# Optimization experiments

Measured on AMD Instinct MI355X. Metric: run time of the kernel, lower is better.

The kernel has to match this reference:

```python
import jax, jax.numpy as jnp
import numpy as np


def setup_inputs() -> dict:
    key = jax.random.key(0)
    B, C, A, P, N = 4, 1, 180, 384, 256
    sinogram = jax.random.normal(key, (B, C, A, P), dtype=jnp.float32)
    # projection angles uniformly covering [0, pi)
    thetas = jnp.linspace(0.0, np.pi, A, endpoint=False).astype(jnp.float32)
    # uniformly spaced detector positions centered at 0, unit spacing
    positions = jnp.arange(P, dtype=jnp.float32) - (P - 1) / 2.0
    return {"sinogram": sinogram, "thetas": thetas, "positions": positions, "image_size": N}


def reference(sinogram, thetas, positions, image_size):
    """Radon backprojection: image[y,x] = sum_a interp(sinogram[a], x*cos+y*sin)."""
    B, C, A, P = sinogram.shape
    N = image_size
    # pixel-center coordinates, image centered at origin (y axis pointing up)
    c = jnp.arange(N, dtype=sinogram.dtype) - (N - 1) / 2.0
    xs = c[None, :]          # [1, N]
    ys = -c[:, None]         # [N, 1]
    cos = jnp.cos(thetas)[:, None, None]  # [A, 1, 1]
    sin = jnp.sin(thetas)[:, None, None]
    t = xs[None] * cos + ys[None] * sin   # [A, N, N] detector coordinate per (angle, pixel)
    # fractional index into the (uniform) detector position grid
    dp = positions[1] - positions[0]
    f = (t - positions[0]) / dp           # [A, N, N]
    i0 = jnp.floor(f)
    w = f - i0                            # linear interpolation weight
    valid = (i0 >= 0) & (i0 <= P - 2)     # rays falling inside the detector
    i0c = jnp.clip(i0, 0, P - 2).astype(jnp.int32)
    idx = i0c.reshape(A, N * N)[None, None]          # [1, 1, A, N*N]
    v0 = jnp.take_along_axis(sinogram, idx, axis=3)  # [B, C, A, N*N]
    v1 = jnp.take_along_axis(sinogram, idx + 1, axis=3)
    wf = w.reshape(A, N * N)[None, None]
    vm = valid.reshape(A, N * N)[None, None]
    val = jnp.where(vm, v0 * (1.0 - wf) + v1 * wf, 0.0)
    return val.sum(axis=2).reshape(B, C, N, N)
```

## Files before the change

### kernel.cpp

```cpp
#include <hip/hip_runtime.h>
#include <hip/hip_fp16.h>
#include <cmath>


#define ACHUNKS 8
#define MAXPE   512

__global__ __launch_bounds__(256) void radon_pack(
    const float* __restrict__ sino,
    const float* __restrict__ thetas,
    const float* __restrict__ positions,
    uint4* __restrict__ packed,
    float2* __restrict__ trig,
    int A, int P, int PE, int bstride)
{
    const int idx = blockIdx.x * 256 + threadIdx.x;
    const int a = idx / PE;
    const int i = idx - a * PE;
    if (a >= A) return;

    const float p0     = positions[0];
    const float inv_dp = 1.0f / (positions[1] - p0);
    if (i == 0) {
        float th = thetas[a];
        trig[a] = make_float2(cosf(th) * inv_dp, sinf(th) * inv_dp);
        if (a == 0) trig[A] = make_float2(-p0 * inv_dp, 0.0f);
    }

    const int i0 = min(i, P - 1);
    const int i1 = min(i + 1, P - 1);
    const float* s = sino + (size_t)a * P;

    uint4 e;
    unsigned* ep = (unsigned*)&e;
#pragma unroll
    for (int b = 0; b < 4; ++b) {
        const float* sb = s + (size_t)b * bstride;
        __half2 h = __floats2half2_rn(sb[i0], sb[i1]);
        ep[b] = *(const unsigned*)&h;
    }
    packed[(size_t)a * PE + i] = e;
}

__global__ __launch_bounds__(256) void radon_partial_gg(
    const uint4* __restrict__ packed,
    const float2* __restrict__ trig,
    float* __restrict__ part,
    int A, int P, int PE, int N, int chunk)
{
    const int tid = threadIdx.x;
    const int nn  = N * N;
    const int pix = blockIdx.x * 256 + tid;
    const int a0  = blockIdx.y * chunk;
    const int cnt = min(A, a0 + chunk) - a0;

    const int x = pix % N;
    const int y = pix / N;
    const float half = (float)(N - 1) * 0.5f;
    const float cx = (float)x - half;
    const float cy = half - (float)y;
    const float q0 = trig[A].x;

    float acc0 = 0.f, acc1 = 0.f, acc2 = 0.f, acc3 = 0.f;

#pragma unroll 4
    for (int i = 0; i < cnt; ++i) {
        const int a = a0 + i;
        float2 t  = trig[a];
        float f   = fmaf(cx, t.x, fmaf(cy, t.y, q0));
        float i0f = floorf(f);
        int   i0  = (int)i0f;
        float w   = f - i0f;
        float m   = (i0 >= 0 && i0 <= P - 2) ? 1.0f : 0.0f;
        int   ic  = min(max(i0, 0), P - 2);
        float wm  = w * m;
        float om  = m - wm;

        uint4 e = packed[(size_t)a * PE + ic];
        const __half2* hp = (const __half2*)&e;
        float2 g0 = __half22float2(hp[0]);
        float2 g1 = __half22float2(hp[1]);
        float2 g2 = __half22float2(hp[2]);
        float2 g3 = __half22float2(hp[3]);
        acc0 = fmaf(om, g0.x, fmaf(wm, g0.y, acc0));
        acc1 = fmaf(om, g1.x, fmaf(wm, g1.y, acc1));
        acc2 = fmaf(om, g2.x, fmaf(wm, g2.y, acc2));
        acc3 = fmaf(om, g3.x, fmaf(wm, g3.y, acc3));
    }

    if (pix < nn) {
        float* pp = part + (size_t)blockIdx.y * 4 * nn + pix;
        pp[0]              = acc0;
        pp[(size_t)nn]     = acc1;
        pp[(size_t)2 * nn] = acc2;
        pp[(size_t)3 * nn] = acc3;
    }
}

__global__ __launch_bounds__(256) void radon_reduce_kernel(
    const float4* __restrict__ part,
    float4* __restrict__ out,
    int BN4, int nchunks)
{
    int i = blockIdx.x * blockDim.x + threadIdx.x;
    if (i >= BN4) return;
    float4 s = make_float4(0.f, 0.f, 0.f, 0.f);
    for (int c = 0; c < nchunks; ++c) {
        float4 v = part[(size_t)c * BN4 + i];
        s.x += v.x; s.y += v.y; s.z += v.z; s.w += v.w;
    }
    out[i] = s;
}

__global__ __launch_bounds__(256) void radon_direct_kernel(
    const float* __restrict__ sino,
    const float* __restrict__ thetas,
    const float* __restrict__ positions,
    float* __restrict__ out,
    int A, int P, int N, int BC)
{
    const int nn  = N * N;
    const int pix = blockIdx.x * blockDim.x + threadIdx.x;
    if (pix >= nn) return;
    const float p0     = positions[0];
    const float inv_dp = 1.0f / (positions[1] - p0);
    const int x = pix % N;
    const int y = pix / N;
    const float half = (float)(N - 1) * 0.5f;
    const float cx = (float)x - half;
    const float cy = half - (float)y;
    for (int b = 0; b < BC; ++b) {
        float acc = 0.0f;
        for (int a = 0; a < A; ++a) {
            float th = thetas[a];
            float f  = (cx * cosf(th) + cy * sinf(th) - p0) * inv_dp;
            float i0f = floorf(f);
            int i0 = (int)i0f;
            float w = f - i0f;
            float m = (i0 >= 0 && i0 <= P - 2) ? 1.0f : 0.0f;
            int ic = min(max(i0, 0), P - 2);
            const float* row = sino + ((size_t)b * A + a) * P + ic;
            acc = fmaf(m, fmaf(w, row[1] - row[0], row[0]), acc);
        }
        out[(size_t)b * nn + pix] = acc;
    }
}

extern "C" void kernel_launch(void* const* d_in, const int* in_sizes, int n_in,
                              void* d_out, int out_size, void* d_ws, size_t ws_size,
                              hipStream_t stream) {
    const float* sino      = (const float*)d_in[0];
    const float* thetas    = (const float*)d_in[1];
    const float* positions = (const float*)d_in[2];
    float* out             = (float*)d_out;

    const int A  = in_sizes[1];
    const int P  = in_sizes[2];
    const int BC = in_sizes[0] / (A * P);
    const int N  = (int)lroundf(sqrtf((float)(out_size / BC)));
    const int nn = N * N;
    const int bstride = A * P;

    const int PE    = (P + 63) & ~63;
    const int chunk = (A + ACHUNKS - 1) / ACHUNKS;

    const size_t part_bytes   = (size_t)ACHUNKS * 4 * nn * sizeof(float);
    const size_t packed_bytes = (size_t)A * PE * sizeof(uint4);
    const size_t trig_bytes   = (size_t)(A + 1) * sizeof(float2);
    const size_t need = part_bytes + packed_bytes + trig_bytes;

    const bool fast = (BC == 4) && (A <= 256) && (P >= 2) && (PE <= MAXPE)
                   && (N % 64 == 0) && ((nn & 255) == 0) && (ws_size >= need);

    if (fast) {
        float*  part   = (float*)d_ws;
        uint4*  packed = (uint4*)((char*)d_ws + part_bytes);
        float2* trig   = (float2*)((char*)d_ws + part_bytes + packed_bytes);

        dim3 block(256);
        dim3 gpack(((unsigned)(A * PE) + 255) / 256);
        radon_pack<<<gpack, block, 0, stream>>>(
            sino, thetas, positions, packed, trig, A, P, PE, bstride);

        dim3 gpart(nn / 256, ACHUNKS);
        radon_partial_gg<<<gpart, block, 0, stream>>>(
            packed, trig, part, A, P, PE, N, chunk);

        const int BN4 = 4 * nn / 4;
        dim3 gred((BN4 + 255) / 256);
        radon_reduce_kernel<<<gred, block, 0, stream>>>(
            (const float4*)part, (float4*)out, BN4, ACHUNKS);
    } else {
        dim3 block(256);
        dim3 grid((nn + 255) / 256);
        radon_direct_kernel<<<grid, block, 0, stream>>>(
            sino, thetas, positions, out, A, P, N, BC);
    }
}
```

Before: 77.68 us.

## Drop angle-chunk split and reduce pass; pad packed table and use fdot2

The gather kernel now loops over all angles in a single pass and writes the output directly, which removes the partial-sum buffer and the separate reduction kernel. The packed sinogram gets a zero sentinel entry at each end, so out-of-range rays land on zeros and the validity mask goes away. The interpolation uses packed fp16 weights with the fdot2 builtin. In exchange the grid shrinks to 256 blocks, which lowers parallelism on a GPU with many CUs, and the weights are now rounded to fp16, which costs some accuracy.

After: 86.74 us. +11.7%, slower.

```diff
diff --git a/kernel.cpp b/kernel.cpp
--- a/kernel.cpp
+++ b/kernel.cpp
@@ -3,8 +3,11 @@
 #include <cmath>
 
 
-#define ACHUNKS 8
-#define MAXPE   512
+typedef __fp16 half2v __attribute__((ext_vector_type(2)));
+
+__device__ __forceinline__ half2v as_h2(unsigned u) {
+    union { unsigned u; half2v h; } x; x.u = u; return x.h;
+}
 
 __global__ __launch_bounds__(256) void radon_pack(
     const float* __restrict__ sino,
@@ -12,47 +15,44 @@
     const float* __restrict__ positions,
     uint4* __restrict__ packed,
     float2* __restrict__ trig,
-    int A, int P, int PE, int bstride)
+    int A, int P, int PES, int bstride)
 {
     const int idx = blockIdx.x * 256 + threadIdx.x;
-    const int a = idx / PE;
-    const int i = idx - a * PE;
+    const int a = idx / PES;
+    const int j = idx - a * PES;
     if (a >= A) return;
 
     const float p0     = positions[0];
     const float inv_dp = 1.0f / (positions[1] - p0);
-    if (i == 0) {
+    if (j == 0) {
         float th = thetas[a];
         trig[a] = make_float2(cosf(th) * inv_dp, sinf(th) * inv_dp);
         if (a == 0) trig[A] = make_float2(-p0 * inv_dp, 0.0f);
     }
 
-    const int i0 = min(i, P - 1);
-    const int i1 = min(i + 1, P - 1);
-    const float* s = sino + (size_t)a * P;
-
-    uint4 e;
-    unsigned* ep = (unsigned*)&e;
+    uint4 e = make_uint4(0, 0, 0, 0);
+    if (j >= 1 && j <= P - 1) {
+        const float* s = sino + (size_t)a * P;
+        unsigned* ep = (unsigned*)&e;
 #pragma unroll
-    for (int b = 0; b < 4; ++b) {
-        const float* sb = s + (size_t)b * bstride;
-        __half2 h = __floats2half2_rn(sb[i0], sb[i1]);
-        ep[b] = *(const unsigned*)&h;
+        for (int b = 0; b < 4; ++b) {
+            const float* sb = s + (size_t)b * bstride;
+            __half2 h = __floats2half2_rn(sb[j - 1], sb[j]);
+            ep[b] = *(const unsigned*)&h;
+        }
     }
-    packed[(size_t)a * PE + i] = e;
+    packed[(size_t)a * PES + j] = e;
 }
 
-__global__ __launch_bounds__(256) void radon_partial_gg(
+__global__ __launch_bounds__(256) void radon_gather(
     const uint4* __restrict__ packed,
     const float2* __restrict__ trig,
-    float* __restrict__ part,
-    int A, int P, int PE, int N, int chunk)
+    float* __restrict__ out,
+    int A, int P, int PES, int N)
 {
     const int tid = threadIdx.x;
     const int nn  = N * N;
     const int pix = blockIdx.x * 256 + tid;
-    const int a0  = blockIdx.y * chunk;
-    const int cnt = min(A, a0 + chunk) - a0;
 
     const int x = pix % N;
     const int y = pix / N;
@@ -64,52 +64,29 @@
     float acc0 = 0.f, acc1 = 0.f, acc2 = 0.f, acc3 = 0.f;
 
 #pragma unroll 4
-    for (int i = 0; i < cnt; ++i) {
-        const int a = a0 + i;
+    for (int a = 0; a < A; ++a) {
         float2 t  = trig[a];
         float f   = fmaf(cx, t.x, fmaf(cy, t.y, q0));
         float i0f = floorf(f);
+        float w   = f - i0f;
         int   i0  = (int)i0f;
-        float w   = f - i0f;
-        float m   = (i0 >= 0 && i0 <= P - 2) ? 1.0f : 0.0f;
-        int   ic  = min(max(i0, 0), P - 2);
-        float wm  = w * m;
-        float om  = m - wm;
+        int   j   = min(max(i0, -1), P - 1) + 1;
 
-        uint4 e = packed[(size_t)a * PE + ic];
-        const __half2* hp = (const __half2*)&e;
-        float2 g0 = __half22float2(hp[0]);
-        float2 g1 = __half22float2(hp[1]);
-        float2 g2 = __half22float2(hp[2]);
-        float2 g3 = __half22float2(hp[3]);
-        acc0 = fmaf(om, g0.x, fmaf(wm, g0.y, acc0));
-        acc1 = fmaf(om, g1.x, fmaf(wm, g1.y, acc1));
-        acc2 = fmaf(om, g2.x, fmaf(wm, g2.y, acc2));
-        acc3 = fmaf(om, g3.x, fmaf(wm, g3.y, acc3));
+        half2v w2 = __builtin_amdgcn_cvt_pkrtz(1.0f - w, w);
+        uint4 e = packed[(size_t)a * PES + j];
+        acc0 = __builtin_amdgcn_fdot2(as_h2(e.x), w2, acc0, false);
+        acc1 = __builtin_amdgcn_fdot2(as_h2(e.y), w2, acc1, false);
+        acc2 = __builtin_amdgcn_fdot2(as_h2(e.z), w2, acc2, false);
+        acc3 = __builtin_amdgcn_fdot2(as_h2(e.w), w2, acc3, false);
     }
 
     if (pix < nn) {
-        float* pp = part + (size_t)blockIdx.y * 4 * nn + pix;
-        pp[0]              = acc0;
-        pp[(size_t)nn]     = acc1;
-        pp[(size_t)2 * nn] = acc2;
-        pp[(size_t)3 * nn] = acc3;
+        float* op = out + pix;
+        op[0]              = acc0;
+        op[(size_t)nn]     = acc1;
+        op[(size_t)2 * nn] = acc2;
+        op[(size_t)3 * nn] = acc3;
     }
-}
-
-__global__ __launch_bounds__(256) void radon_reduce_kernel(
-    const float4* __restrict__ part,
-    float4* __restrict__ out,
-    int BN4, int nchunks)
-{
-    int i = blockIdx.x * blockDim.x + threadIdx.x;
-    if (i >= BN4) return;
-    float4 s = make_float4(0.f, 0.f, 0.f, 0.f);
-    for (int c = 0; c < nchunks; ++c) {
-        float4 v = part[(size_t)c * BN4 + i];
-        s.x += v.x; s.y += v.y; s.z += v.z; s.w += v.w;
-    }
-    out[i] = s;
 }
 
 __global__ __launch_bounds__(256) void radon_direct_kernel(
@@ -161,35 +138,27 @@
     const int nn = N * N;
     const int bstride = A * P;
 
-    const int PE    = (P + 63) & ~63;
-    const int chunk = (A + ACHUNKS - 1) / ACHUNKS;
+    const int PES = (P + 2 + 63) & ~63;
 
-    const size_t part_bytes   = (size_t)ACHUNKS * 4 * nn * sizeof(float);
-    const size_t packed_bytes = (size_t)A * PE * sizeof(uint4);
+    const size_t packed_bytes = (size_t)A * PES * sizeof(uint4);
     const size_t trig_bytes   = (size_t)(A + 1) * sizeof(float2);
-    const size_t need = part_bytes + packed_bytes + trig_bytes;
+    const size_t need = packed_bytes + trig_bytes;
 
-    const bool fast = (BC == 4) && (A <= 256) && (P >= 2) && (PE <= MAXPE)
-                   && (N % 64 == 0) && ((nn & 255) == 0) && (ws_size >= need);
+    const bool fast = (BC == 4) && (A <= 1024) && (P >= 2)
+                   && ((nn & 255) == 0) && (ws_size >= need);
 
     if (fast) {
-        float*  part   = (float*)d_ws;
-        uint4*  packed = (uint4*)((char*)d_ws + part_bytes);
-        float2* trig   = (float2*)((char*)d_ws + part_bytes + packed_bytes);
+        uint4*  packed = (uint4*)d_ws;
+        float2* trig   = (float2*)((char*)d_ws + packed_bytes);
 
         dim3 block(256);
-        dim3 gpack(((unsigned)(A * PE) + 255) / 256);
+        dim3 gpack(((unsigned)(A * PES) + 255) / 256);
         radon_pack<<<gpack, block, 0, stream>>>(
-            sino, thetas, positions, packed, trig, A, P, PE, bstride);
+            sino, thetas, positions, packed, trig, A, P, PES, bstride);
 
-        dim3 gpart(nn / 256, ACHUNKS);
-        radon_partial_gg<<<gpart, block, 0, stream>>>(
-            packed, trig, part, A, P, PE, N, chunk);
-
-        const int BN4 = 4 * nn / 4;
-        dim3 gred((BN4 + 255) / 256);
-        radon_reduce_kernel<<<gred, block, 0, stream>>>(
-            (const float4*)part, (float4*)out, BN4, ACHUNKS);
+        dim3 ggat(nn / 256);
+        radon_gather<<<ggat, block, 0, stream>>>(
+            packed, trig, out, A, P, PES, N);
     } else {
         dim3 block(256);
         dim3 grid((nn + 255) / 256);
```
